# Performance work log

Measured on AMD Instinct MI355X. Metric: run time of the kernel, lower is better.

## Reference

```python
import jax, jax.numpy as jnp
import numpy as np
from jax import lax

B, IN_N, OUT_N, SEQ, HID = 8, 16, 16, 256, 64
NUM_C = 64 + 3  # grid_size + spline_order
EPS_LN = 1e-5


def setup_inputs():
    key = jax.random.key(0)
    k = jax.random.split(key, 8)
    f32 = jnp.float32
    return {
        "x_in": jax.random.normal(k[0], (B, IN_N, SEQ, HID), f32),
        "proj_x_prev": jax.random.normal(k[1], (B, IN_N, SEQ, HID), f32),
        "spline_weights": jax.random.normal(k[2], (IN_N, OUT_N, NUM_C), f32) * 0.1,
        "base_scales": 0.6 + 0.1 * jax.random.normal(k[3], (IN_N, OUT_N), f32),
        "tau": jax.random.normal(k[4], (IN_N, OUT_N), f32) * 0.1 + 0.1,
        "temperature": jnp.array(1.0, f32),
        "omiga": jnp.full((IN_N, OUT_N), 0.2, f32),
        "W2": jax.random.normal(k[5], (OUT_N, HID, HID), f32) / np.sqrt(HID).astype(np.float32),
        "b_param": jnp.zeros((OUT_N, SEQ, HID), f32),
        "ln_w": jnp.ones((OUT_N, HID), f32),
        "ln_b": jnp.zeros((OUT_N, HID), f32),
        "alpha": jnp.full((OUT_N,), 0.5, f32),
        "beta": jnp.ones((OUT_N,), f32),
        "gamma": jnp.full((OUT_N,), 0.5, f32),
        "theta": jnp.ones((OUT_N,), f32),
        "conv_w": jax.random.normal(k[6], (OUT_N, HID, 1, 3, 3), f32) * 0.1,
    }


def _layernorm(x, w=None, b=None):
    mu = jnp.mean(x, -1, keepdims=True)
    var = jnp.mean((x - mu) ** 2, -1, keepdims=True)
    y = (x - mu) / jnp.sqrt(var + EPS_LN)
    if w is not None:
        y = y * w + b
    return y


def _dwconv(x, w):
    # x: [b, C, 16, 16]; w: [C, 1, 3, 3]; depthwise conv, SAME padding
    return lax.conv_general_dilated(
        x, w, (1, 1), "SAME",
        dimension_numbers=("NCHW", "OIHW", "NCHW"),
        feature_group_count=x.shape[1])


def _forward(x_in, proj_x_prev, spline_weights, base_scales, tau, temperature,
             omiga, W2, b_param, ln_w, ln_b, alpha, beta, gamma, theta, conv_w):
    b, in_n, seq, feat = x_in.shape
    num_c = spline_weights.shape[-1]
    grid = jnp.linspace(-1.0, 1.0, num_c)
    h = 2.0 / (num_c - 1)

    x_energy = jnp.mean(x_in, -1)  # [b,i,s]
    x_norm = jnp.clip(
        x_energy / (jnp.max(jnp.abs(x_energy), -1, keepdims=True) + 1e-8),
        -0.99, 0.99)

    # cubic B-spline basis (masked branches -> nested where)
    dist = jnp.abs(x_norm[..., None] - grid) / h  # [b,i,s,c]
    basis = jnp.where(dist < 1.0, 2.0 / 3.0 - dist ** 2 + dist ** 3 / 2.0,
            jnp.where(dist < 2.0, (2.0 - dist) ** 3 / 6.0, jnp.zeros_like(dist)))

    base_feat = jax.nn.silu(x_norm)[:, :, None, :] * base_scales[None, :, :, None]  # [b,i,j,s]
    spline_feat = jnp.einsum("bisc,ijc->bijs", basis, spline_weights)
    edge_resp = base_feat + spline_feat
    # [b,i,j,s,f]
    activated = (edge_resp[..., None] + jnp.abs(omiga)[None, :, :, None, None]) * x_in[:, :, None]

    t_val = jnp.abs(temperature) + 1e-4
    edge_energies = jnp.mean(jnp.abs(activated), axis=(-1, -2))  # [b,i,j]
    tau_abs = jnp.abs(tau)  # [i,j]
    mask = jax.nn.sigmoid((edge_energies - tau_abs[None]) / t_val)  # [b,i,j]

    # attention kernel W1, vectorized over output neuron j
    mid = in_n // 2
    mult = edge_energies / (tau_abs[None] + 1e-8)  # [b,i,j]
    wp = proj_x_prev[:, :, None] * (mult * mask)[..., None, None]  # [b,i,j,s,d]
    d = wp.shape[-1]
    K = jnp.transpose(wp[:, :mid], (0, 2, 3, 1, 4)).reshape(b, -1, seq, mid * d)
    Q = jnp.transpose(wp[:, mid:2 * mid], (0, 2, 3, 1, 4)).reshape(b, -1, seq, mid * d)
    K, Q = _layernorm(K), _layernorm(Q)
    raw = jnp.einsum("bjsk,bjtk->bjst", K, Q) / (jnp.sqrt(jnp.float32(mid * d)) * t_val)
    W1 = jax.nn.softmax(raw, axis=-1)  # [b,j,s,s]

    # masked mean over input neurons -> per-neuron SplineWeightLayer (vectorized)
    x = jnp.mean(activated * mask[..., None, None], axis=1)  # [b,j,s,f]
    xn = _layernorm(x, ln_w[None, :, None, :], ln_b[None, :, None, :])
    x_prime = jnp.einsum("bjsf,jfo->bjso", xn, W2) + b_param[None]  # [b,j,s,o]
    o = x_prime.shape[-1]

    # depthwise 3x3 conv on 16x16 spatial view, per-j kernels
    xsp = jnp.transpose(x_prime, (1, 0, 3, 2)).reshape(-1, b, o, 16, 16)  # [j,b,o,16,16]
    w3 = jax.vmap(_dwconv)(xsp, conv_w)  # [j,b,o,16,16]
    w3 = jnp.transpose(w3.reshape(-1, b, o, seq), (1, 0, 3, 2))  # [b,j,s,o]

    eye = jnp.eye(seq, dtype=x_prime.dtype)
    ak = (jnp.abs(beta)[None, :, None, None] * W1
          + jnp.abs(alpha)[None, :, None, None] * eye[None, None])
    glob = jnp.einsum("bjst,bjto->bjso", ak, x_prime)
    combined = glob + jnp.abs(theta)[None, :, None, None] * w3
    # residual_proj is Identity since in_hidden == out_hidden
    out = combined + gamma[None, :, None, None] * x
    return out, x_prime  # both [b, out_n, seq, out_hidden]


def reference(x_in, proj_x_prev, spline_weights, base_scales, tau, temperature,
              omiga, W2, b_param, ln_w, ln_b, alpha, beta, gamma, theta, conv_w):
    return _forward(x_in, proj_x_prev, spline_weights, base_scales, tau, temperature,
                    omiga, W2, b_param, ln_w, ln_b, alpha, beta, gamma, theta, conv_w)
```

## Files before the change

kernel.cpp:

```cpp
#include <hip/hip_runtime.h>

#define EPSLN 1e-5f

typedef short bf16x8 __attribute__((ext_vector_type(8)));
typedef float f32x4 __attribute__((ext_vector_type(4)));
typedef unsigned short u16;
typedef unsigned short u16x8 __attribute__((ext_vector_type(8)));

__device__ __forceinline__ float wsum(float v){
  #pragma unroll
  for(int o=32;o;o>>=1) v += __shfl_xor(v,o);
  return v;
}
__device__ __forceinline__ float wmax(float v){
  #pragma unroll
  for(int o=32;o;o>>=1) v = fmaxf(v,__shfl_xor(v,o));
  return v;
}
__device__ __forceinline__ u16 f2bf(float f){
  unsigned int u = __float_as_uint(f);
  u = (u + 0x7FFFu + ((u>>16)&1u)) >> 16;
  return (u16)u;
}
__device__ __forceinline__ float bf2f(u16 h){
  return __uint_as_float(((unsigned int)h)<<16);
}

__global__ void __launch_bounds__(256) kA(
                   const float* __restrict__ xin, const float* __restrict__ p,
                   const float* __restrict__ W2,
                   float* __restrict__ xe, float* __restrict__ xa,
                   float* __restrict__ Sv, float* __restrict__ SSv,
                   u16* __restrict__ xinb, u16* __restrict__ phi, u16* __restrict__ plo,
                   u16* __restrict__ w2B){
  int t = threadIdx.x;
  int rl = t>>3, q = t&7;
  int row = blockIdx.x*32 + rl;
  const float4* xr = (const float4*)(xin + row*64 + q*8);
  const float4* pr = (const float4*)(p   + row*64 + q*8);
  float s1=0.f,s2=0.f,s3=0.f,s4=0.f;
  u16x8 xb, ph, pl;
  #pragma unroll
  for(int k=0;k<2;k++){
    float4 xv = xr[k];
    float4 pv = pr[k];
    s1 += xv.x+xv.y+xv.z+xv.w;
    s2 += fabsf(xv.x)+fabsf(xv.y)+fabsf(xv.z)+fabsf(xv.w);
    s3 += pv.x+pv.y+pv.z+pv.w;
    s4 += pv.x*pv.x+pv.y*pv.y+pv.z*pv.z+pv.w*pv.w;
    int o = k*4;
    xb[o+0]=f2bf(xv.x); xb[o+1]=f2bf(xv.y); xb[o+2]=f2bf(xv.z); xb[o+3]=f2bf(xv.w);
    u16 h0=f2bf(pv.x), h1=f2bf(pv.y), h2=f2bf(pv.z), h3=f2bf(pv.w);
    ph[o+0]=h0; ph[o+1]=h1; ph[o+2]=h2; ph[o+3]=h3;
    pl[o+0]=f2bf(pv.x-bf2f(h0)); pl[o+1]=f2bf(pv.y-bf2f(h1));
    pl[o+2]=f2bf(pv.z-bf2f(h2)); pl[o+3]=f2bf(pv.w-bf2f(h3));
  }
  *(u16x8*)(xinb + row*64 + q*8) = xb;
  *(u16x8*)(phi  + row*64 + q*8) = ph;
  *(u16x8*)(plo  + row*64 + q*8) = pl;
  s1 += __shfl_xor(s1,1); s1 += __shfl_xor(s1,2); s1 += __shfl_xor(s1,4);
  s2 += __shfl_xor(s2,1); s2 += __shfl_xor(s2,2); s2 += __shfl_xor(s2,4);
  s3 += __shfl_xor(s3,1); s3 += __shfl_xor(s3,2); s3 += __shfl_xor(s3,4);
  s4 += __shfl_xor(s4,1); s4 += __shfl_xor(s4,2); s4 += __shfl_xor(s4,4);
  if(q==0){ xe[row]=s1*(1.f/64.f); xa[row]=s2*(1.f/64.f); Sv[row]=s3; SSv[row]=s4; }
  if(blockIdx.x<16){
    int j = blockIdx.x;
    for(int idx=threadIdx.x; idx<4096; idx+=256){
      int f = idx>>6, o = idx&63;
      float v = W2[j*4096 + idx];
      int ks = f>>5, kb = (f>>3)&3, i = f&7;
      int nt = o>>4, col = o&15;
      int ln = kb*16 + col;
      w2B[((j*2+ks)*4 + nt)*512 + ln*8 + i] = f2bf(v);
    }
  }
}

__global__ void __launch_bounds__(256) kBE(
                   const float* __restrict__ xe, const float* __restrict__ sw,
                   const float* __restrict__ bs, const float* __restrict__ om,
                   const float* __restrict__ xa, const float* __restrict__ tau,
                   const float* __restrict__ temp,
                   float* __restrict__ er2, float* __restrict__ mask,
                   float* __restrict__ cc,
                   const u16* __restrict__ phi, const u16* __restrict__ plo,
                   float* __restrict__ G){
  __shared__ __align__(16) unsigned char shm[32768];
  int tid = threadIdx.x;
  if(blockIdx.x < 128){
    float* swL = (float*)shm;
    float* bsL = swL + 1072;
    float* omL = bsL + 16;
    float* red = omL + 16;
    float* redE= red + 4;
    int bi = blockIdx.x;
    int i = bi & 15;
    int w = tid>>6, lane = tid&63;
    for(int k=tid;k<16*67;k+=256) swL[k] = sw[i*16*67 + k];
    if(tid<16){ bsL[tid]=bs[i*16+tid]; omL[tid]=fabsf(om[i*16+tid]); }
    float v = xe[bi*256+tid];
    float m = wmax(fabsf(v));
    if(lane==0) red[w]=m;
    __syncthreads();
    m = fmaxf(fmaxf(red[0],red[1]),fmaxf(red[2],red[3]));
    float xn = v/(m+1e-8f);
    xn = fminf(fmaxf(xn,-0.99f),0.99f);
    float sil = xn/(1.f+expf(-xn));
    float vv = (xn+1.f)*33.f;
    int c0 = (int)floorf(vv)-1;
    float acc[16];
    #pragma unroll
    for(int j=0;j<16;j++) acc[j]=0.f;
    #pragma unroll
    for(int k=0;k<4;k++){
      int c = c0+k;
      if(c<0||c>66) continue;
      float d = fabsf(vv-(float)c);
      float bas = d<1.f ? (2.f/3.f - d*d + d*d*d*0.5f)
                : (d<2.f ? (2.f-d)*(2.f-d)*(2.f-d)*(1.f/6.f) : 0.f);
      #pragma unroll
      for(int j=0;j<16;j++) acc[j] += bas*swL[j*67+c];
    }
    float xav = xa[bi*256+tid];
    #pragma unroll
    for(int j=0;j<16;j++){
      float ev = sil*bsL[j] + acc[j] + omL[j];
      er2[(bi*16+j)*256+tid] = ev;
      float pe = wsum(fabsf(ev)*xav);
      if(lane==0) redE[j*4+w]=pe;
    }
    __syncthreads();
    if(tid<16){
      float e = (redE[tid*4+0]+redE[tid*4+1]+redE[tid*4+2]+redE[tid*4+3])*(1.f/256.f);
      float tv = fabsf(temp[0])+1e-4f;
      float ta = fabsf(tau[i*16+tid]);
      float mk = 1.f/(1.f+expf(-(e-ta)/tv));
      mask[bi*16+tid]=mk;
      cc[bi*16+tid]= e/(ta+1e-8f)*mk;
    }
  } else {
    u16* AfB = (u16*)shm;
    u16* BfB = AfB + 8192;
    int e = blockIdx.x - 128;
    int b = e&7, m = (e>>3)&7, sx = (e>>6)&3, ty = e>>8;
    int bm = b*8+m;
    int s0 = sx*64, t0 = ty*64;
    int row = tid>>2, dseg = tid&3;
    size_t offA = ((size_t)(b*16+m  )*256 + s0 + row)*64 + dseg*16;
    size_t offB = ((size_t)(b*16+m+8)*256 + t0 + row)*64 + dseg*16;
    int d0 = dseg*16;
    int ks0 = d0>>5, kb0 = (d0>>3)&3;
    int ks1 = (d0+8)>>5, kb1 = ((d0+8)>>3)&3;
    int lr = row&15, stile = row>>4;
    #define AOFF(h,stl,ks,ln) (((((h)*4+(stl))*2+(ks))*64 + (ln))*8)
    {
      uint4 v0 = *(const uint4*)(phi + offA);
      uint4 v1 = *(const uint4*)(phi + offA + 8);
      *(uint4*)(AfB + AOFF(0,stile,ks0,kb0*16+lr)) = v0;
      *(uint4*)(AfB + AOFF(0,stile,ks1,kb1*16+lr)) = v1;
      uint4 w0 = *(const uint4*)(plo + offA);
      uint4 w1 = *(const uint4*)(plo + offA + 8);
      *(uint4*)(AfB + AOFF(1,stile,ks0,kb0*16+lr)) = w0;
      *(uint4*)(AfB + AOFF(1,stile,ks1,kb1*16+lr)) = w1;
      uint4 x0 = *(const uint4*)(phi + offB);
      uint4 x1 = *(const uint4*)(phi + offB + 8);
      *(uint4*)(BfB + AOFF(0,stile,ks0,kb0*16+lr)) = x0;
      *(uint4*)(BfB + AOFF(0,stile,ks1,kb1*16+lr)) = x1;
      uint4 y0 = *(const uint4*)(plo + offB);
      uint4 y1 = *(const uint4*)(plo + offB + 8);
      *(uint4*)(BfB + AOFF(1,stile,ks0,kb0*16+lr)) = y0;
      *(uint4*)(BfB + AOFF(1,stile,ks1,kb1*16+lr)) = y1;
    }
    __syncthreads();
    int w = tid>>6, lane = tid&63;
    bf16x8 ah0 = *(const bf16x8*)(AfB + AOFF(0,w,0,lane));
    bf16x8 ah1 = *(const bf16x8*)(AfB + AOFF(0,w,1,lane));
    bf16x8 al0 = *(const bf16x8*)(AfB + AOFF(1,w,0,lane));
    bf16x8 al1 = *(const bf16x8*)(AfB + AOFF(1,w,1,lane));
    f32x4 acc[4];
    #pragma unroll
    for(int tt=0;tt<4;tt++) acc[tt] = (f32x4){0.f,0.f,0.f,0.f};
    #pragma unroll
    for(int tt=0;tt<4;tt++){
      bf16x8 bh0 = *(const bf16x8*)(BfB + AOFF(0,tt,0,lane));
      bf16x8 bh1 = *(const bf16x8*)(BfB + AOFF(0,tt,1,lane));
      bf16x8 bl0 = *(const bf16x8*)(BfB + AOFF(1,tt,0,lane));
      bf16x8 bl1 = *(const bf16x8*)(BfB + AOFF(1,tt,1,lane));
      acc[tt] = __builtin_amdgcn_mfma_f32_16x16x32_bf16(ah0, bh0, acc[tt], 0,0,0);
      acc[tt] = __builtin_amdgcn_mfma_f32_16x16x32_bf16(ah1, bh1, acc[tt], 0,0,0);
      acc[tt] = __builtin_amdgcn_mfma_f32_16x16x32_bf16(ah0, bl0, acc[tt], 0,0,0);
      acc[tt] = __builtin_amdgcn_mfma_f32_16x16x32_bf16(ah1, bl1, acc[tt], 0,0,0);
      acc[tt] = __builtin_amdgcn_mfma_f32_16x16x32_bf16(al0, bh0, acc[tt], 0,0,0);
      acc[tt] = __builtin_amdgcn_mfma_f32_16x16x32_bf16(al1, bh1, acc[tt], 0,0,0);
    }
    int col = lane&15, r4 = lane>>4;
    #pragma unroll
    for(int tt=0;tt<4;tt++){
      #pragma unroll
      for(int r=0;r<4;r++){
        G[((size_t)bm*256 + s0 + w*16 + r4*4 + r)*256 + t0 + tt*16 + col] = acc[tt][r];
      }
    }
    #undef AOFF
  }
}

__global__ void __launch_bounds__(256) kD(
                   const u16* __restrict__ xinb, const float* __restrict__ er2,
                   const float* __restrict__ mask, const u16* __restrict__ w2B,
                   const float* __restrict__ lnw, const float* __restrict__ lnb,
                   const float* __restrict__ bp,
                   u16* __restrict__ xoutb, float* __restrict__ xp,
                   u16* __restrict__ xpB){
  int b = blockIdx.x, j = blockIdx.y, st = blockIdx.z;
  int tid = threadIdx.x, w = tid>>6, lane = tid&63;
  __shared__ __align__(16) u16 xnS[16*64];
  __shared__ float mcL[16];
  if(tid<16) mcL[tid]=mask[(b*16+tid)*16+j];
  __syncthreads();
  int bj = b*16+j;
  unsigned char* xnB = (unsigned char*)xnS;
  int ss = lane>>4, fq = lane&15;
  int sl = w*4 + ss;
  int s  = st*16 + sl;
  float4 lw4 = *(const float4*)(lnw + j*64 + fq*4);
  float4 lb4 = *(const float4*)(lnb + j*64 + fq*4);
  float acc0=0.f,acc1=0.f,acc2=0.f,acc3=0.f;
  #pragma unroll
  for(int i=0;i<16;i++){
    float er = er2[((b*16+i)*16+j)*256+s]*mcL[i];
    ushort4 xv = *(const ushort4*)(xinb + ((size_t)(b*16+i)*256+s)*64 + fq*4);
    acc0 += er*bf2f(xv.x);
    acc1 += er*bf2f(xv.y);
    acc2 += er*bf2f(xv.z);
    acc3 += er*bf2f(xv.w);
  }
  acc0*=(1.f/16.f); acc1*=(1.f/16.f); acc2*=(1.f/16.f); acc3*=(1.f/16.f);
  {
    u16 pk[4]={f2bf(acc0),f2bf(acc1),f2bf(acc2),f2bf(acc3)};
    *(ushort4*)(xoutb + ((size_t)bj*256+s)*64 + fq*4) = *(ushort4*)pk;
  }
  float part = acc0+acc1+acc2+acc3;
  part += __shfl_xor(part,1); part += __shfl_xor(part,2);
  part += __shfl_xor(part,4); part += __shfl_xor(part,8);
  float mu = part*(1.f/64.f);
  float d0=acc0-mu, d1=acc1-mu, d2=acc2-mu, d3=acc3-mu;
  float p2 = d0*d0+d1*d1+d2*d2+d3*d3;
  p2 += __shfl_xor(p2,1); p2 += __shfl_xor(p2,2);
  p2 += __shfl_xor(p2,4); p2 += __shfl_xor(p2,8);
  float rstd = rsqrtf(p2*(1.f/64.f)+EPSLN);
  {
    u16 xn[4] = { f2bf(d0*rstd*lw4.x + lb4.x), f2bf(d1*rstd*lw4.y + lb4.y),
                  f2bf(d2*rstd*lw4.z + lb4.z), f2bf(d3*rstd*lw4.w + lb4.w) };
    *(ushort4*)(xnB + ((sl*128 + fq*8) ^ ((sl&7)<<4))) = *(ushort4*)xn;
  }
  __syncthreads();
  f32x4 acc = {0.f,0.f,0.f,0.f};
  int m = lane&15, kb = lane>>4;
  #pragma unroll
  for(int ks=0;ks<2;ks++){
    bf16x8 a = *(const bf16x8*)(xnB + ((m*128 + ks*64 + kb*16) ^ ((m&7)<<4)));
    bf16x8 bfr = *(const bf16x8*)(w2B + ((j*2+ks)*4 + w)*512 + lane*8);
    acc = __builtin_amdgcn_mfma_f32_16x16x32_bf16(a, bfr, acc, 0, 0, 0);
  }
  int f = w*16 + m;
  u16 pk[4];
  #pragma unroll
  for(int r=0;r<4;r++){
    int si = kb*4 + r;
    int s2 = st*16 + si;
    float xpr = acc[r] + bp[((size_t)j*256+s2)*64+f];
    xp[((size_t)bj*256+s2)*64+f] = xpr;
    pk[r] = f2bf(xpr);
  }
  int s0 = st*16 + kb*4;
  int flat = ((s0>>5)*4 + w)*512 + ((s0>>3)&3)*128 + m*8 + (s0&7);
  *(ushort4*)(xpB + (size_t)bj*16384 + flat) = *(ushort4*)pk;
}

__global__ void __launch_bounds__(256) kF(
    const float* __restrict__ G, const float* __restrict__ cc,
    const float* __restrict__ Sv, const float* __restrict__ SSv,
    const float* __restrict__ xp, const u16* __restrict__ xpB,
    const float* __restrict__ cw,
    const u16* __restrict__ xarrb, const float* __restrict__ temp,
    const float* __restrict__ alpha, const float* __restrict__ beta,
    const float* __restrict__ gamma_, const float* __restrict__ theta,
    float* __restrict__ out){
  int b = blockIdx.x, jp = blockIdx.y, st = blockIdx.z;
  int j0 = jp*2, j1 = j0+1;
  int tid = threadIdx.x, w = tid>>6, lane = tid&63;
  __shared__ __align__(16) unsigned char ovl[26112];
  unsigned char* prB0 = ovl;
  unsigned char* prB1 = ovl + 8192;
  float* mQL0 = (float*)(ovl + 16384);
  float* rQL0 = (float*)(ovl + 17408);
  float* mQL1 = (float*)(ovl + 18432);
  float* rQL1 = (float*)(ovl + 19456);
  float* mK2  = (float*)(ovl + 20480);
  float* rK2  = (float*)(ovl + 20608);
  float* xpT  = (float*)ovl;
  float tv = fabsf(temp[0])+1e-4f;
  float inv = 1.f/(sqrtf(512.f)*tv);
  float ck0[8],cq0[8],ck1[8],cq1[8],aM0[8],aM1[8];
  #pragma unroll
  for(int m=0;m<8;m++){
    ck0[m]=cc[(b*16+m)*16+j0];  cq0[m]=cc[(b*16+m+8)*16+j0];
    ck1[m]=cc[(b*16+m)*16+j1];  cq1[m]=cc[(b*16+m+8)*16+j1];
    aM0[m]=ck0[m]*cq0[m];       aM1[m]=ck1[m]*cq1[m];
  }
  {
    int t = tid;
    float sk0=0,ssk0=0,sq0=0,ssq0=0,sk1=0,ssk1=0,sq1=0,ssq1=0;
    #pragma unroll
    for(int m=0;m<8;m++){
      float svk = Sv [(b*16+m)*256+t];
      float ssvk= SSv[(b*16+m)*256+t];
      float svq = Sv [(b*16+m+8)*256+t];
      float ssvq= SSv[(b*16+m+8)*256+t];
      sk0 += ck0[m]*svk;  ssk0 += ck0[m]*ck0[m]*ssvk;
      sq0 += cq0[m]*svq;  ssq0 += cq0[m]*cq0[m]*ssvq;
      sk1 += ck1[m]*svk;  ssk1 += ck1[m]*ck1[m]*ssvk;
      sq1 += cq1[m]*svq;  ssq1 += cq1[m]*cq1[m]*ssvq;
    }
    float mq0 = sq0*(1.f/512.f), mq1 = sq1*(1.f/512.f);
    mQL0[t]=mq0; rQL0[t]=rsqrtf(ssq0*(1.f/512.f)-mq0*mq0+EPSLN);
    mQL1[t]=mq1; rQL1[t]=rsqrtf(ssq1*(1.f/512.f)-mq1*mq1+EPSLN);
    if((t>>4)==st){
      int si = t&15;
      float mk0 = sk0*(1.f/512.f), mk1 = sk1*(1.f/512.f);
      mK2[si]   =mk0; rK2[si]   =rsqrtf(ssk0*(1.f/512.f)-mk0*mk0+EPSLN);
      mK2[16+si]=mk1; rK2[16+si]=rsqrtf(ssk1*(1.f/512.f)-mk1*mk1+EPSLN);
    }
  }
  __syncthreads();
  int bj0 = b*16+j0, bj1 = b*16+j1;
  const float* Gb = G + (size_t)(b*8)*65536;
  float4 mQ40 = *(const float4*)&mQL0[lane*4];
  float4 rQ40 = *(const float4*)&rQL0[lane*4];
  float4 mQ41 = *(const float4*)&mQL1[lane*4];
  float4 rQ41 = *(const float4*)&rQL1[lane*4];
  #pragma unroll
  for(int q=0;q<4;q++){
    int si = w*4+q;
    int s = st*16 + si;
    f32x4 dot0 = {0.f,0.f,0.f,0.f}, dot1 = {0.f,0.f,0.f,0.f};
    #pragma unroll
    for(int m=0;m<8;m++){
      f32x4 g4 = *(const f32x4*)(Gb + (size_t)m*65536 + s*256 + lane*4);
      dot0 += aM0[m]*g4;
      dot1 += aM1[m]*g4;
    }
    {
      float mKs = 512.f*mK2[si], rKs = rK2[si];
      float e0 = expf((dot0[0] - mKs*mQ40.x)*rKs*rQ40.x*inv);
      float e1 = expf((dot0[1] - mKs*mQ40.y)*rKs*rQ40.y*inv);
      float e2 = expf((dot0[2] - mKs*mQ40.z)*rKs*rQ40.z*inv);
      float e3 = expf((dot0[3] - mKs*mQ40.w)*rKs*rQ40.w*inv);
      float isf = 1.f/wsum(e0+e1+e2+e3);
      u16 pk[4] = {f2bf(e0*isf), f2bf(e1*isf), f2bf(e2*isf), f2bf(e3*isf)};
      *(ushort4*)(prB0 + ((si*512 + lane*8) ^ ((si&7)<<4))) = *(ushort4*)pk;
    }
    {
      float mKs = 512.f*mK2[16+si], rKs = rK2[16+si];
      float e0 = expf((dot1[0] - mKs*mQ41.x)*rKs*rQ41.x*inv);
      float e1 = expf((dot1[1] - mKs*mQ41.y)*rKs*rQ41.y*inv);
      float e2 = expf((dot1[2] - mKs*mQ41.z)*rKs*rQ41.z*inv);
      float e3 = expf((dot1[3] - mKs*mQ41.w)*rKs*rQ41.w*inv);
      float isf = 1.f/wsum(e0+e1+e2+e3);
      u16 pk[4] = {f2bf(e0*isf), f2bf(e1*isf), f2bf(e2*isf), f2bf(e3*isf)};
      *(ushort4*)(prB1 + ((si*512 + lane*8) ^ ((si&7)<<4))) = *(ushort4*)pk;
    }
  }
  __syncthreads();
  int m_ = lane&15, kb = lane>>4;
  f32x4 acc0 = {0.f,0.f,0.f,0.f}, acc1 = {0.f,0.f,0.f,0.f};
  const u16* xpB0 = xpB + (size_t)bj0*16384;
  const u16* xpB1 = xpB + (size_t)bj1*16384;
  #pragma unroll
  for(int ks=0;ks<8;ks++){
    int aoff = (m_*512 + ks*64 + kb*16) ^ ((m_&7)<<4);
    int boff = ((ks*4 + w)*64 + lane)*8;
    bf16x8 a0 = *(const bf16x8*)(prB0 + aoff);
    bf16x8 a1 = *(const bf16x8*)(prB1 + aoff);
    acc0 = __builtin_amdgcn_mfma_f32_16x16x32_bf16(a0, *(const bf16x8*)(xpB0 + boff), acc0, 0,0,0);
    acc1 = __builtin_amdgcn_mfma_f32_16x16x32_bf16(a1, *(const bf16x8*)(xpB1 + boff), acc1, 0,0,0);
  }
  __syncthreads();
  for(int idx4 = tid; idx4 < 1536; idx4 += 256){
    int jj = idx4 / 768;
    int rem = idx4 - jj*768;
    int rr_i = rem >> 8;
    int pos = rem & 255;
    int ci = pos>>4, f4 = pos&15;
    int grow = st - 1 + rr_i;
    float4 v = {0.f,0.f,0.f,0.f};
    if(grow>=0 && grow<16){
      v = *(const float4*)(xp + ((size_t)(b*16+j0+jj)*256 + grow*16 + ci)*64 + f4*4);
    }
    *(float4*)(xpT + ((jj*3+rr_i)*16+ci)*68 + f4*4) = v;
  }
  __syncthreads();
  int f = w*16 + m_;
  #pragma unroll
  for(int jj=0;jj<2;jj++){
    int j = j0+jj;
    int bj = b*16+j;
    f32x4 acc = jj ? acc1 : acc0;
    float al = fabsf(alpha[j]), be=fabsf(beta[j]), th=fabsf(theta[j]), ga=gamma_[j];
    const float* wq = cw + (j*64+f)*9;
    float w0=wq[0],w1=wq[1],w2=wq[2],w3v=wq[3],w4=wq[4],w5=wq[5],w6=wq[6],w7=wq[7],w8=wq[8];
    #pragma unroll
    for(int r=0;r<4;r++){
      int si = kb*4 + r;
      int s = st*16 + si;
      float gl = acc[r];
      float cv=0.f;
      #pragma unroll
      for(int dr=0;dr<3;dr++){
        float kw0 = dr==0?w0:(dr==1?w3v:w6);
        float kw1 = dr==0?w1:(dr==1?w4:w7);
        float kw2 = dr==0?w2:(dr==1?w5:w8);
        const float* rowp = xpT + ((jj*3+dr)*16)*68;
        if(si>0)  cv += rowp[(si-1)*68+f]*kw0;
                  cv += rowp[(si  )*68+f]*kw1;
        if(si<15) cv += rowp[(si+1)*68+f]*kw2;
      }
      float diag = xpT[((jj*3+1)*16+si)*68+f];
      size_t gi = ((size_t)bj*256+s)*64+f;
      out[gi] = be*gl + al*diag + th*cv + ga*bf2f(xarrb[gi]);
    }
  }
}

extern "C" void kernel_launch(void* const* d_in, const int* in_sizes, int n_in,
                              void* d_out, int out_size, void* d_ws, size_t ws_size,
                              hipStream_t stream) {
  const float* xin = (const float*)d_in[0];
  const float* pxp = (const float*)d_in[1];
  const float* sw  = (const float*)d_in[2];
  const float* bs  = (const float*)d_in[3];
  const float* tau = (const float*)d_in[4];
  const float* temp= (const float*)d_in[5];
  const float* om  = (const float*)d_in[6];
  const float* W2  = (const float*)d_in[7];
  const float* bp  = (const float*)d_in[8];
  const float* lnw = (const float*)d_in[9];
  const float* lnb = (const float*)d_in[10];
  const float* alpha=(const float*)d_in[11];
  const float* beta= (const float*)d_in[12];
  const float* gam = (const float*)d_in[13];
  const float* theta=(const float*)d_in[14];
  const float* cw  = (const float*)d_in[15];
  float* outp = (float*)d_out;
  float* xpo  = outp + 2097152;

  float* ws  = (float*)d_ws;
  float* xe  = ws;
  float* xa  = xe + 32768;
  float* Sv  = xa + 32768;
  float* SSv = Sv + 32768;
  float* er2 = SSv + 32768;
  float* mask= er2 + 524288;
  float* ccv = mask + 2048;
  float* Gv  = ccv + 2048;
  u16* xvb = (u16*)(Gv + 4194304);
  u16* xpB = xvb + 2097152;
  u16* w2B = xpB + 2097152;
  u16* xinb= w2B + 65536;
  u16* phi = xinb + 2097152;
  u16* plo = phi + 2097152;

  kA<<<1024,256,0,stream>>>(xin,pxp,W2,xe,xa,Sv,SSv,xinb,phi,plo,w2B);
  kBE<<<1152,256,0,stream>>>(xe,sw,bs,om,xa,tau,temp,er2,mask,ccv,phi,plo,Gv);
  kD<<<dim3(8,16,16),256,0,stream>>>(xinb,er2,mask,w2B,lnw,lnb,bp,xvb,xpo,xpB);
  kF<<<dim3(8,8,16),256,0,stream>>>(Gv,ccv,Sv,SSv,xpo,xpB,cw,xvb,temp,
                                    alpha,beta,gam,theta,outp);
}
```

Baseline: 58.00 us.

## Process four output channels per block in kF to reuse G loads

Each kF block now handles four j channels instead of two, so every G tile read from global memory feeds four attention dot products. The grid shrinks to 512 blocks, shared memory grows to about 41 KB, and the conv/epilogue stage runs in two passes that reuse the xpT staging buffer. expf is also swapped for the faster, less precise __expf. The trade-off is fewer blocks in flight, higher register pressure and lower occupancy on a 256-CU device.

```diff
diff --git a/kernel.cpp b/kernel.cpp
--- a/kernel.cpp
+++ b/kernel.cpp
@@ -288,147 +288,157 @@
     const float* __restrict__ gamma_, const float* __restrict__ theta,
     float* __restrict__ out){
   int b = blockIdx.x, jp = blockIdx.y, st = blockIdx.z;
-  int j0 = jp*2, j1 = j0+1;
+  int j0 = jp*4;
   int tid = threadIdx.x, w = tid>>6, lane = tid&63;
-  __shared__ __align__(16) unsigned char ovl[26112];
-  unsigned char* prB0 = ovl;
-  unsigned char* prB1 = ovl + 8192;
-  float* mQL0 = (float*)(ovl + 16384);
-  float* rQL0 = (float*)(ovl + 17408);
-  float* mQL1 = (float*)(ovl + 18432);
-  float* rQL1 = (float*)(ovl + 19456);
-  float* mK2  = (float*)(ovl + 20480);
-  float* rK2  = (float*)(ovl + 20608);
-  float* xpT  = (float*)ovl;
+  __shared__ __align__(16) unsigned char ovl[41472];
+  float* mQL = (float*)(ovl + 32768);
+  float* rQL = (float*)(ovl + 36864);
+  float* mKL = (float*)(ovl + 40960);
+  float* rKL = (float*)(ovl + 41216);
+  float* xpT = (float*)ovl;
   float tv = fabsf(temp[0])+1e-4f;
   float inv = 1.f/(sqrtf(512.f)*tv);
-  float ck0[8],cq0[8],ck1[8],cq1[8],aM0[8],aM1[8];
-  #pragma unroll
-  for(int m=0;m<8;m++){
-    ck0[m]=cc[(b*16+m)*16+j0];  cq0[m]=cc[(b*16+m+8)*16+j0];
-    ck1[m]=cc[(b*16+m)*16+j1];  cq1[m]=cc[(b*16+m+8)*16+j1];
-    aM0[m]=ck0[m]*cq0[m];       aM1[m]=ck1[m]*cq1[m];
-  }
+  float aM0[8],aM1[8],aM2[8],aM3[8];
   {
     int t = tid;
-    float sk0=0,ssk0=0,sq0=0,ssq0=0,sk1=0,ssk1=0,sq1=0,ssq1=0;
+    float sk0=0,sk1=0,sk2=0,sk3=0, ssk0=0,ssk1=0,ssk2=0,ssk3=0;
+    float sq0=0,sq1=0,sq2=0,sq3=0, ssq0=0,ssq1=0,ssq2=0,ssq3=0;
     #pragma unroll
     for(int m=0;m<8;m++){
+      float4 ck = *(const float4*)(cc + (b*16+m  )*16 + j0);
+      float4 cq = *(const float4*)(cc + (b*16+m+8)*16 + j0);
+      aM0[m]=ck.x*cq.x; aM1[m]=ck.y*cq.y; aM2[m]=ck.z*cq.z; aM3[m]=ck.w*cq.w;
       float svk = Sv [(b*16+m)*256+t];
       float ssvk= SSv[(b*16+m)*256+t];
       float svq = Sv [(b*16+m+8)*256+t];
       float ssvq= SSv[(b*16+m+8)*256+t];
-      sk0 += ck0[m]*svk;  ssk0 += ck0[m]*ck0[m]*ssvk;
-      sq0 += cq0[m]*svq;  ssq0 += cq0[m]*cq0[m]*ssvq;
-      sk1 += ck1[m]*svk;  ssk1 += ck1[m]*ck1[m]*ssvk;
-      sq1 += cq1[m]*svq;  ssq1 += cq1[m]*cq1[m]*ssvq;
-    }
-    float mq0 = sq0*(1.f/512.f), mq1 = sq1*(1.f/512.f);
-    mQL0[t]=mq0; rQL0[t]=rsqrtf(ssq0*(1.f/512.f)-mq0*mq0+EPSLN);
-    mQL1[t]=mq1; rQL1[t]=rsqrtf(ssq1*(1.f/512.f)-mq1*mq1+EPSLN);
+      sk0 += ck.x*svk; ssk0 += ck.x*ck.x*ssvk;
+      sk1 += ck.y*svk; ssk1 += ck.y*ck.y*ssvk;
+      sk2 += ck.z*svk; ssk2 += ck.z*ck.z*ssvk;
+      sk3 += ck.w*svk; ssk3 += ck.w*ck.w*ssvk;
+      sq0 += cq.x*svq; ssq0 += cq.x*cq.x*ssvq;
+      sq1 += cq.y*svq; ssq1 += cq.y*cq.y*ssvq;
+      sq2 += cq.z*svq; ssq2 += cq.z*cq.z*ssvq;
+      sq3 += cq.w*svq; ssq3 += cq.w*cq.w*ssvq;
+    }
+    float mq;
+    mq = sq0*(1.f/512.f); mQL[0*256+t]=mq; rQL[0*256+t]=rsqrtf(ssq0*(1.f/512.f)-mq*mq+EPSLN);
+    mq = sq1*(1.f/512.f); mQL[1*256+t]=mq; rQL[1*256+t]=rsqrtf(ssq1*(1.f/512.f)-mq*mq+EPSLN);
+    mq = sq2*(1.f/512.f); mQL[2*256+t]=mq; rQL[2*256+t]=rsqrtf(ssq2*(1.f/512.f)-mq*mq+EPSLN);
+    mq = sq3*(1.f/512.f); mQL[3*256+t]=mq; rQL[3*256+t]=rsqrtf(ssq3*(1.f/512.f)-mq*mq+EPSLN);
     if((t>>4)==st){
       int si = t&15;
-      float mk0 = sk0*(1.f/512.f), mk1 = sk1*(1.f/512.f);
-      mK2[si]   =mk0; rK2[si]   =rsqrtf(ssk0*(1.f/512.f)-mk0*mk0+EPSLN);
-      mK2[16+si]=mk1; rK2[16+si]=rsqrtf(ssk1*(1.f/512.f)-mk1*mk1+EPSLN);
+      float mk;
+      mk = sk0*(1.f/512.f); mKL[0*16+si]=mk; rKL[0*16+si]=rsqrtf(ssk0*(1.f/512.f)-mk*mk+EPSLN);
+      mk = sk1*(1.f/512.f); mKL[1*16+si]=mk; rKL[1*16+si]=rsqrtf(ssk1*(1.f/512.f)-mk*mk+EPSLN);
+      mk = sk2*(1.f/512.f); mKL[2*16+si]=mk; rKL[2*16+si]=rsqrtf(ssk2*(1.f/512.f)-mk*mk+EPSLN);
+      mk = sk3*(1.f/512.f); mKL[3*16+si]=mk; rKL[3*16+si]=rsqrtf(ssk3*(1.f/512.f)-mk*mk+EPSLN);
     }
   }
   __syncthreads();
-  int bj0 = b*16+j0, bj1 = b*16+j1;
   const float* Gb = G + (size_t)(b*8)*65536;
-  float4 mQ40 = *(const float4*)&mQL0[lane*4];
-  float4 rQ40 = *(const float4*)&rQL0[lane*4];
-  float4 mQ41 = *(const float4*)&mQL1[lane*4];
-  float4 rQ41 = *(const float4*)&rQL1[lane*4];
+  float4 mQ4a = *(const float4*)&mQL[0*256+lane*4];
+  float4 rQ4a = *(const float4*)&rQL[0*256+lane*4];
+  float4 mQ4b = *(const float4*)&mQL[1*256+lane*4];
+  float4 rQ4b = *(const float4*)&rQL[1*256+lane*4];
+  float4 mQ4c = *(const float4*)&mQL[2*256+lane*4];
+  float4 rQ4c = *(const float4*)&rQL[2*256+lane*4];
+  float4 mQ4d = *(const float4*)&mQL[3*256+lane*4];
+  float4 rQ4d = *(const float4*)&rQL[3*256+lane*4];
   #pragma unroll
   for(int q=0;q<4;q++){
     int si = w*4+q;
     int s = st*16 + si;
-    f32x4 dot0 = {0.f,0.f,0.f,0.f}, dot1 = {0.f,0.f,0.f,0.f};
+    f32x4 dt0={0.f,0.f,0.f,0.f}, dt1={0.f,0.f,0.f,0.f};
+    f32x4 dt2={0.f,0.f,0.f,0.f}, dt3={0.f,0.f,0.f,0.f};
     #pragma unroll
     for(int m=0;m<8;m++){
       f32x4 g4 = *(const f32x4*)(Gb + (size_t)m*65536 + s*256 + lane*4);
-      dot0 += aM0[m]*g4;
-      dot1 += aM1[m]*g4;
-    }
-    {
-      float mKs = 512.f*mK2[si], rKs = rK2[si];
-      float e0 = expf((dot0[0] - mKs*mQ40.x)*rKs*rQ40.x*inv);
-      float e1 = expf((dot0[1] - mKs*mQ40.y)*rKs*rQ40.y*inv);
-      float e2 = expf((dot0[2] - mKs*mQ40.z)*rKs*rQ40.z*inv);
-      float e3 = expf((dot0[3] - mKs*mQ40.w)*rKs*rQ40.w*inv);
-      float isf = 1.f/wsum(e0+e1+e2+e3);
-      u16 pk[4] = {f2bf(e0*isf), f2bf(e1*isf), f2bf(e2*isf), f2bf(e3*isf)};
-      *(ushort4*)(prB0 + ((si*512 + lane*8) ^ ((si&7)<<4))) = *(ushort4*)pk;
-    }
-    {
-      float mKs = 512.f*mK2[16+si], rKs = rK2[16+si];
-      float e0 = expf((dot1[0] - mKs*mQ41.x)*rKs*rQ41.x*inv);
-      float e1 = expf((dot1[1] - mKs*mQ41.y)*rKs*rQ41.y*inv);
-      float e2 = expf((dot1[2] - mKs*mQ41.z)*rKs*rQ41.z*inv);
-      float e3 = expf((dot1[3] - mKs*mQ41.w)*rKs*rQ41.w*inv);
-      float isf = 1.f/wsum(e0+e1+e2+e3);
-      u16 pk[4] = {f2bf(e0*isf), f2bf(e1*isf), f2bf(e2*isf), f2bf(e3*isf)};
-      *(ushort4*)(prB1 + ((si*512 + lane*8) ^ ((si&7)<<4))) = *(ushort4*)pk;
-    }
+      dt0 += aM0[m]*g4; dt1 += aM1[m]*g4;
+      dt2 += aM2[m]*g4; dt3 += aM3[m]*g4;
+    }
+    #define SMAX(JJ, DT, MQ, RQ) { \
+      float mKs = 512.f*mKL[JJ*16+si], rKs = rKL[JJ*16+si]; \
+      float e0 = __expf((DT[0] - mKs*MQ.x)*rKs*RQ.x*inv); \
+      float e1 = __expf((DT[1] - mKs*MQ.y)*rKs*RQ.y*inv); \
+      float e2 = __expf((DT[2] - mKs*MQ.z)*rKs*RQ.z*inv); \
+      float e3 = __expf((DT[3] - mKs*MQ.w)*rKs*RQ.w*inv); \
+      float isf = 1.f/wsum(e0+e1+e2+e3); \
+      u16 pk[4] = {f2bf(e0*isf), f2bf(e1*isf), f2bf(e2*isf), f2bf(e3*isf)}; \
+      *(ushort4*)(ovl + JJ*8192 + ((si*512 + lane*8) ^ ((si&7)<<4))) = *(ushort4*)pk; }
+    SMAX(0, dt0, mQ4a, rQ4a)
+    SMAX(1, dt1, mQ4b, rQ4b)
+    SMAX(2, dt2, mQ4c, rQ4c)
+    SMAX(3, dt3, mQ4d, rQ4d)
+    #undef SMAX
   }
   __syncthreads();
   int m_ = lane&15, kb = lane>>4;
-  f32x4 acc0 = {0.f,0.f,0.f,0.f}, acc1 = {0.f,0.f,0.f,0.f};
-  const u16* xpB0 = xpB + (size_t)bj0*16384;
-  const u16* xpB1 = xpB + (size_t)bj1*16384;
+  f32x4 av0={0.f,0.f,0.f,0.f}, av1={0.f,0.f,0.f,0.f};
+  f32x4 av2={0.f,0.f,0.f,0.f}, av3={0.f,0.f,0.f,0.f};
+  const u16* xpB0 = xpB + (size_t)(b*16+j0  )*16384;
+  const u16* xpB1 = xpB + (size_t)(b*16+j0+1)*16384;
+  const u16* xpB2 = xpB + (size_t)(b*16+j0+2)*16384;
+  const u16* xpB3 = xpB + (size_t)(b*16+j0+3)*16384;
   #pragma unroll
   for(int ks=0;ks<8;ks++){
     int aoff = (m_*512 + ks*64 + kb*16) ^ ((m_&7)<<4);
     int boff = ((ks*4 + w)*64 + lane)*8;
-    bf16x8 a0 = *(const bf16x8*)(prB0 + aoff);
-    bf16x8 a1 = *(const bf16x8*)(prB1 + aoff);
-    acc0 = __builtin_amdgcn_mfma_f32_16x16x32_bf16(a0, *(const bf16x8*)(xpB0 + boff), acc0, 0,0,0);
-    acc1 = __builtin_amdgcn_mfma_f32_16x16x32_bf16(a1, *(const bf16x8*)(xpB1 + boff), acc1, 0,0,0);
-  }
-  __syncthreads();
-  for(int idx4 = tid; idx4 < 1536; idx4 += 256){
-    int jj = idx4 / 768;
-    int rem = idx4 - jj*768;
-    int rr_i = rem >> 8;
-    int pos = rem & 255;
-    int ci = pos>>4, f4 = pos&15;
-    int grow = st - 1 + rr_i;
-    float4 v = {0.f,0.f,0.f,0.f};
-    if(grow>=0 && grow<16){
-      v = *(const float4*)(xp + ((size_t)(b*16+j0+jj)*256 + grow*16 + ci)*64 + f4*4);
-    }
-    *(float4*)(xpT + ((jj*3+rr_i)*16+ci)*68 + f4*4) = v;
-  }
-  __syncthreads();
+    bf16x8 a0 = *(const bf16x8*)(ovl +         aoff);
+    bf16x8 a1 = *(const bf16x8*)(ovl +  8192 + aoff);
+    bf16x8 a2 = *(const bf16x8*)(ovl + 16384 + aoff);
+    bf16x8 a3 = *(const bf16x8*)(ovl + 24576 + aoff);
+    av0 = __builtin_amdgcn_mfma_f32_16x16x32_bf16(a0, *(const bf16x8*)(xpB0 + boff), av0, 0,0,0);
+    av1 = __builtin_amdgcn_mfma_f32_16x16x32_bf16(a1, *(const bf16x8*)(xpB1 + boff), av1, 0,0,0);
+    av2 = __builtin_amdgcn_mfma_f32_16x16x32_bf16(a2, *(const bf16x8*)(xpB2 + boff), av2, 0,0,0);
+    av3 = __builtin_amdgcn_mfma_f32_16x16x32_bf16(a3, *(const bf16x8*)(xpB3 + boff), av3, 0,0,0);
+  }
   int f = w*16 + m_;
   #pragma unroll
-  for(int jj=0;jj<2;jj++){
-    int j = j0+jj;
-    int bj = b*16+j;
-    f32x4 acc = jj ? acc1 : acc0;
-    float al = fabsf(alpha[j]), be=fabsf(beta[j]), th=fabsf(theta[j]), ga=gamma_[j];
-    const float* wq = cw + (j*64+f)*9;
-    float w0=wq[0],w1=wq[1],w2=wq[2],w3v=wq[3],w4=wq[4],w5=wq[5],w6=wq[6],w7=wq[7],w8=wq[8];
-    #pragma unroll
-    for(int r=0;r<4;r++){
-      int si = kb*4 + r;
-      int s = st*16 + si;
-      float gl = acc[r];
-      float cv=0.f;
+  for(int pass=0; pass<2; pass++){
+    __syncthreads();
+    for(int idx4 = tid; idx4 < 1536; idx4 += 256){
+      int jj = idx4 / 768;
+      int rem = idx4 - jj*768;
+      int rr_i = rem >> 8;
+      int pos = rem & 255;
+      int ci = pos>>4, f4 = pos&15;
+      int grow = st - 1 + rr_i;
+      float4 v = {0.f,0.f,0.f,0.f};
+      if(grow>=0 && grow<16){
+        v = *(const float4*)(xp + ((size_t)(b*16+j0+pass*2+jj)*256 + grow*16 + ci)*64 + f4*4);
+      }
+      *(float4*)(xpT + ((jj*3+rr_i)*16+ci)*68 + f4*4) = v;
+    }
+    __syncthreads();
+    #pragma unroll
+    for(int jj=0;jj<2;jj++){
+      int j = j0 + pass*2 + jj;
+      int bj = b*16+j;
+      f32x4 acc = pass==0 ? (jj?av1:av0) : (jj?av3:av2);
+      float al = fabsf(alpha[j]), be=fabsf(beta[j]), th=fabsf(theta[j]), ga=gamma_[j];
+      const float* wq = cw + (j*64+f)*9;
+      float w0=wq[0],w1=wq[1],w2=wq[2],w3v=wq[3],w4=wq[4],w5=wq[5],w6=wq[6],w7=wq[7],w8=wq[8];
       #pragma unroll
-      for(int dr=0;dr<3;dr++){
-        float kw0 = dr==0?w0:(dr==1?w3v:w6);
-        float kw1 = dr==0?w1:(dr==1?w4:w7);
-        float kw2 = dr==0?w2:(dr==1?w5:w8);
-        const float* rowp = xpT + ((jj*3+dr)*16)*68;
-        if(si>0)  cv += rowp[(si-1)*68+f]*kw0;
-                  cv += rowp[(si  )*68+f]*kw1;
-        if(si<15) cv += rowp[(si+1)*68+f]*kw2;
+      for(int r=0;r<4;r++){
+        int si = kb*4 + r;
+        int s = st*16 + si;
+        float gl = acc[r];
+        float cv=0.f;
+        #pragma unroll
+        for(int dr=0;dr<3;dr++){
+          float kw0 = dr==0?w0:(dr==1?w3v:w6);
+          float kw1 = dr==0?w1:(dr==1?w4:w7);
+          float kw2 = dr==0?w2:(dr==1?w5:w8);
+          const float* rowp = xpT + ((jj*3+dr)*16)*68;
+          if(si>0)  cv += rowp[(si-1)*68+f]*kw0;
+                    cv += rowp[(si  )*68+f]*kw1;
+          if(si<15) cv += rowp[(si+1)*68+f]*kw2;
+        }
+        float diag = xpT[((jj*3+1)*16+si)*68+f];
+        size_t gi = ((size_t)bj*256+s)*64+f;
+        out[gi] = be*gl + al*diag + th*cv + ga*bf2f(xarrb[gi]);
       }
-      float diag = xpT[((jj*3+1)*16+si)*68+f];
-      size_t gi = ((size_t)bj*256+s)*64+f;
-      out[gi] = be*gl + al*diag + th*cv + ga*bf2f(xarrb[gi]);
     }
   }
 }
@@ -474,6 +484,6 @@
   kA<<<1024,256,0,stream>>>(xin,pxp,W2,xe,xa,Sv,SSv,xinb,phi,plo,w2B);
   kBE<<<1152,256,0,stream>>>(xe,sw,bs,om,xa,tau,temp,er2,mask,ccv,phi,plo,Gv);
   kD<<<dim3(8,16,16),256,0,stream>>>(xinb,er2,mask,w2B,lnw,lnb,bp,xvb,xpo,xpB);
-  kF<<<dim3(8,8,16),256,0,stream>>>(Gv,ccv,Sv,SSv,xpo,xpB,cw,xvb,temp,
+  kF<<<dim3(8,4,16),256,0,stream>>>(Gv,ccv,Sv,SSv,xpo,xpB,cw,xvb,temp,
                                     alpha,beta,gam,theta,outp);
 }
```

New measurement: 56.47 us. -2.6%, faster.
